# Kernel optimization log

Hardware: AMD Instinct MI355X
Metric: run time of the kernel (lower is better)

The kernel has to match this reference:

```python
import jax, jax.numpy as jnp
import numpy as np

N = 16384
IN_DIM = 128
OUT_DIM = 128
NUM_TYPES = 8


def setup_inputs() -> dict:
    key = jax.random.key(0)
    k1, k2, k3, k4 = jax.random.split(key, 4)
    x = jax.random.normal(k1, (N, IN_DIM), dtype=jnp.float32)
    node_types = jax.random.randint(k2, (N,), 0, NUM_TYPES, dtype=jnp.int32)
    adjacency = jax.random.uniform(k3, (N, N), dtype=jnp.float32)
    weight = jax.random.normal(k4, (NUM_TYPES, OUT_DIM, IN_DIM), dtype=jnp.float32)
    return {"x": x, "node_types": node_types, "adjacency": adjacency, "weight": weight}


def reference(x, node_types, adjacency, weight):
    # agg = A @ x : (N, in_dim)
    agg = jnp.matmul(adjacency, x)
    # Per-type projection: compute agg @ W[t].T for all types, then select
    # by node type. (N, T, out) intermediate is small (N*T*out floats).
    per_type = jnp.einsum("nd,tod->nto", agg, weight)  # (N, T, out)
    out = jnp.take_along_axis(per_type, node_types[:, None, None].astype(jnp.int32), axis=1)
    return out[:, 0, :]  # (N, out)
```

## Files before the change

kernel.cpp:

```cpp
#include <hip/hip_runtime.h>
#include <stdint.h>


#define N_NODES 16384
#define DIM     128
#define NTYPES  8
#define BM      64
#define BK      32
#define NIT     (N_NODES / BK)

typedef float  f32x4  __attribute__((ext_vector_type(4)));
typedef __bf16 bf16x8 __attribute__((ext_vector_type(8)));

__device__ __attribute__((aligned(16))) unsigned short g_xT[DIM * N_NODES];
__device__ __attribute__((aligned(16))) unsigned short g_Wb[NTYPES * DIM * DIM];

__device__ __forceinline__ unsigned int f2b(float f) {
    unsigned int u = __float_as_uint(f);
    u += 0x7FFFu + ((u >> 16) & 1u);
    return u >> 16;
}
#define BF_LO(u) __uint_as_float((unsigned int)(u) << 16)
#define BF_HI(u) __uint_as_float((unsigned int)(u) & 0xFFFF0000u)

__device__ __forceinline__ bf16x8 cvt8(const f32x4 lo, const f32x4 hi) {
    bf16x8 r;
    r[0] = (__bf16)lo[0]; r[1] = (__bf16)lo[1]; r[2] = (__bf16)lo[2]; r[3] = (__bf16)lo[3];
    r[4] = (__bf16)hi[0]; r[5] = (__bf16)hi[1]; r[6] = (__bf16)hi[2]; r[7] = (__bf16)hi[3];
    return r;
}


__global__ void prep_all(const float* __restrict__ x, const float* __restrict__ w) {
    const int tid = threadIdx.x;
    if (blockIdx.x < 64) {
        int n = blockIdx.x * 256 + tid;
        const float* row = x + (size_t)n * DIM;
#pragma unroll
        for (int d0 = 0; d0 < DIM; d0 += 4) {
            float4 v = *(const float4*)(row + d0);
            g_xT[(d0 + 0) * N_NODES + n] = (unsigned short)f2b(v.x);
            g_xT[(d0 + 1) * N_NODES + n] = (unsigned short)f2b(v.y);
            g_xT[(d0 + 2) * N_NODES + n] = (unsigned short)f2b(v.z);
            g_xT[(d0 + 3) * N_NODES + n] = (unsigned short)f2b(v.w);
        }
    } else {
        int base = ((blockIdx.x - 64) * 256 + tid) * 16;
#pragma unroll
        for (int j = 0; j < 4; ++j) {
            float4 v = *(const float4*)(w + base + j * 4);
            ushort4 o;
            o.x = (unsigned short)f2b(v.x); o.y = (unsigned short)f2b(v.y);
            o.z = (unsigned short)f2b(v.z); o.w = (unsigned short)f2b(v.w);
            *(ushort4*)(g_Wb + base + j * 4) = o;
        }
    }
}


#define ABYTES 8192
#define XBYTES 8192

#define GLOAD16(g, l) __builtin_amdgcn_global_load_lds(                         \
    (const __attribute__((address_space(1))) unsigned int*)(g),                 \
    (__attribute__((address_space(3))) unsigned int*)(l), 16, 0, 0)

#define COMPUTE(Ab, Xb) do {                                                    \
    f32x4 _lo = *(const f32x4*)((Ab) + aoE);                                    \
    f32x4 _hi = *(const f32x4*)((Ab) + aoO);                                    \
    bf16x8 _af = cvt8(_lo, _hi);                                                \
    bf16x8 _b0 = *(const bf16x8*)((Xb) + xbase);                                \
    bf16x8 _b1 = *(const bf16x8*)((Xb) + xbase + 1024);                         \
    bf16x8 _b2 = *(const bf16x8*)((Xb) + xbase + 2048);                         \
    bf16x8 _b3 = *(const bf16x8*)((Xb) + xbase + 3072);                         \
    acc0 = __builtin_amdgcn_mfma_f32_16x16x32_bf16(_af, _b0, acc0, 0, 0, 0);    \
    acc1 = __builtin_amdgcn_mfma_f32_16x16x32_bf16(_af, _b1, acc1, 0, 0, 0);    \
    acc2 = __builtin_amdgcn_mfma_f32_16x16x32_bf16(_af, _b2, acc2, 0, 0, 0);    \
    acc3 = __builtin_amdgcn_mfma_f32_16x16x32_bf16(_af, _b3, acc3, 0, 0, 0);    \
} while (0)

#define PHASE_I(Ac, Xc, Ai, Xi, VM) do {                                        \
    asm volatile("s_waitcnt vmcnt(" VM ")" ::: "memory");                       \
    __builtin_amdgcn_s_barrier();                                               \
    GLOAD16(gAp, (Ai) + wq);                                                    \
    GLOAD16(gXp, (Xi) + wq);                                                    \
    gAp += BK; gXp += BK;                                                       \
    COMPUTE(Ac, Xc);                                                            \
} while (0)

#define PHASE_N(Ac, Xc, VM) do {                                                \
    asm volatile("s_waitcnt vmcnt(" VM ")" ::: "memory");                       \
    __builtin_amdgcn_s_barrier();                                               \
    COMPUTE(Ac, Xc);                                                            \
} while (0)

__global__ __launch_bounds__(512, 1) void gconv_main(
    const float* __restrict__ adj,
    const int* __restrict__ types,
    float* __restrict__ out)
{
    __shared__ __align__(16) unsigned char lds[3 * ABYTES + 3 * XBYTES];
    unsigned char* A0 = lds;
    unsigned char* A1 = lds + ABYTES;
    unsigned char* A2 = lds + 2 * ABYTES;
    unsigned char* X0 = lds + 3 * ABYTES;
    unsigned char* X1 = X0 + XBYTES;
    unsigned char* X2 = X0 + 2 * XBYTES;

    const int tid  = threadIdx.x;
    const int w    = tid >> 6;
    const int l    = tid & 63;
    const int m0   = blockIdx.x * BM;

    const int mrow = (w & 3) * 16;
    const int ncol = (w >> 2) * 64;

    f32x4 acc0 = {}, acc1 = {}, acc2 = {}, acc3 = {};

    const float* gAp = adj + (size_t)(m0 + 8 * w + (l >> 3)) * N_NODES
                     + (((l & 7) ^ (l >> 3)) << 2);
    const unsigned short* gXp = g_xT + (size_t)(16 * w + (l >> 2)) * N_NODES
                              + (((l & 3) ^ ((l >> 3) & 3)) << 3);
    const int wq = w << 10;

    const int arow = mrow + (l & 15);
    const int ce   = (l >> 4) << 1;
    const int aoE  = arow * 128 + ((ce ^ (l & 7)) << 4);
    const int aoO  = arow * 128 + (((ce + 1) ^ (l & 7)) << 4);
    const int xph  = (l >> 4) ^ (((l & 15) >> 1) & 3);
    const int xbase = (ncol + (l & 15)) * 64 + (xph << 4);

    GLOAD16(gAp, A0 + wq); GLOAD16(gXp, X0 + wq); gAp += BK; gXp += BK;
    GLOAD16(gAp, A1 + wq); GLOAD16(gXp, X1 + wq); gAp += BK; gXp += BK;

    for (int j = 0; j < 169; ++j) {
        PHASE_I(A0, X0, A2, X2, "2");
        PHASE_I(A1, X1, A0, X0, "2");
        PHASE_I(A2, X2, A1, X1, "2");
    }
    PHASE_I(A0, X0, A2, X2, "2");
    PHASE_I(A1, X1, A0, X0, "2");
    PHASE_I(A2, X2, A1, X1, "2");
    PHASE_N(A0, X0, "2");
    PHASE_N(A1, X1, "0");
    __syncthreads();

    float* agg = (float*)lds;
#pragma unroll
    for (int r = 0; r < 4; ++r) {
        const int gr = (mrow + (l >> 4) * 4 + r) * 132 + ncol + (l & 15);
        agg[gr +  0] = acc0[r];
        agg[gr + 16] = acc1[r];
        agg[gr + 32] = acc2[r];
        agg[gr + 48] = acc3[r];
    }
    __syncthreads();

    const int rbase = w * 8;
    for (int rr = 0; rr < 8; ++rr) {
        const int rw = rbase + rr;
        const int nn = m0 + rw;
        const int ty = types[nn];
        const unsigned short* Wt = g_Wb + ty * (DIM * DIM);
        const int o0 = l * 2;
        const float* aggRow = agg + rw * 132;
        float s0 = 0.f, s1 = 0.f;
#pragma unroll
        for (int d0 = 0; d0 < DIM; d0 += 8) {
            float4 ga = *(const float4*)(aggRow + d0);
            float4 gb = *(const float4*)(aggRow + d0 + 4);
            uint4 wa = *(const uint4*)(Wt + o0 * DIM + d0);
            uint4 wb = *(const uint4*)(Wt + (o0 + 1) * DIM + d0);
            s0 += ga.x * BF_LO(wa.x) + ga.y * BF_HI(wa.x) + ga.z * BF_LO(wa.y) + ga.w * BF_HI(wa.y);
            s0 += gb.x * BF_LO(wa.z) + gb.y * BF_HI(wa.z) + gb.z * BF_LO(wa.w) + gb.w * BF_HI(wa.w);
            s1 += ga.x * BF_LO(wb.x) + ga.y * BF_HI(wb.x) + ga.z * BF_LO(wb.y) + ga.w * BF_HI(wb.y);
            s1 += gb.x * BF_LO(wb.z) + gb.y * BF_HI(wb.z) + gb.z * BF_LO(wb.w) + gb.w * BF_HI(wb.w);
        }
        float2 res; res.x = s0; res.y = s1;
        *(float2*)(out + (size_t)nn * DIM + o0) = res;
    }
}


extern "C" void kernel_launch(void* const* d_in, const int* in_sizes, int n_in,
                              void* d_out, int out_size, void* d_ws, size_t ws_size,
                              hipStream_t stream) {
    const float* x     = (const float*)d_in[0];
    const int*   types = (const int*)d_in[1];
    const float* adj   = (const float*)d_in[2];
    const float* wt    = (const float*)d_in[3];
    float* out = (float*)d_out;

    hipLaunchKernelGGL(prep_all, dim3(96), dim3(256), 0, stream, x, wt);
    hipLaunchKernelGGL(gconv_main, dim3(N_NODES / BM), dim3(512), 0, stream, adj, types, out);
}
```

Before: 350.8 us.

## Widen K tile to 128 with double-buffered LDS and fewer barriers

```diff
diff --git a/kernel.cpp b/kernel.cpp
--- a/kernel.cpp
+++ b/kernel.cpp
@@ -6,8 +6,8 @@
 #define DIM     128
 #define NTYPES  8
 #define BM      64
-#define BK      32
-#define NIT     (N_NODES / BK)
+#define BK      128
+#define NT_K    (N_NODES / BK)
 
 typedef float  f32x4  __attribute__((ext_vector_type(4)));
 typedef __bf16 bf16x8 __attribute__((ext_vector_type(8)));
@@ -58,40 +58,49 @@
 }
 
 
-#define ABYTES 8192
-#define XBYTES 8192
+#define ABYTES 32768
+#define XBYTES 32768
 
 #define GLOAD16(g, l) __builtin_amdgcn_global_load_lds(                         \
     (const __attribute__((address_space(1))) unsigned int*)(g),                 \
     (__attribute__((address_space(3))) unsigned int*)(l), 16, 0, 0)
 
-#define COMPUTE(Ab, Xb) do {                                                    \
-    f32x4 _lo = *(const f32x4*)((Ab) + aoE);                                    \
-    f32x4 _hi = *(const f32x4*)((Ab) + aoO);                                    \
-    bf16x8 _af = cvt8(_lo, _hi);                                                \
-    bf16x8 _b0 = *(const bf16x8*)((Xb) + xbase);                                \
-    bf16x8 _b1 = *(const bf16x8*)((Xb) + xbase + 1024);                         \
-    bf16x8 _b2 = *(const bf16x8*)((Xb) + xbase + 2048);                         \
-    bf16x8 _b3 = *(const bf16x8*)((Xb) + xbase + 3072);                         \
-    acc0 = __builtin_amdgcn_mfma_f32_16x16x32_bf16(_af, _b0, acc0, 0, 0, 0);    \
-    acc1 = __builtin_amdgcn_mfma_f32_16x16x32_bf16(_af, _b1, acc1, 0, 0, 0);    \
-    acc2 = __builtin_amdgcn_mfma_f32_16x16x32_bf16(_af, _b2, acc2, 0, 0, 0);    \
-    acc3 = __builtin_amdgcn_mfma_f32_16x16x32_bf16(_af, _b3, acc3, 0, 0, 0);    \
-} while (0)
-
-#define PHASE_I(Ac, Xc, Ai, Xi, VM) do {                                        \
-    asm volatile("s_waitcnt vmcnt(" VM ")" ::: "memory");                       \
-    __builtin_amdgcn_s_barrier();                                               \
-    GLOAD16(gAp, (Ai) + wq);                                                    \
-    GLOAD16(gXp, (Xi) + wq);                                                    \
-    gAp += BK; gXp += BK;                                                       \
-    COMPUTE(Ac, Xc);                                                            \
-} while (0)
-
-#define PHASE_N(Ac, Xc, VM) do {                                                \
-    asm volatile("s_waitcnt vmcnt(" VM ")" ::: "memory");                       \
-    __builtin_amdgcn_s_barrier();                                               \
-    COMPUTE(Ac, Xc);                                                            \
+#define DMA8(Ab, Xb) do {                                                       \
+    GLOAD16(gA0, (Ab) + wq);          GLOAD16(gA1, (Ab) +  8192 + wq);          \
+    GLOAD16(gA2, (Ab) + 16384 + wq);  GLOAD16(gA3, (Ab) + 24576 + wq);          \
+    GLOAD16(gX0, (Xb) + wq);          GLOAD16(gX1, (Xb) +  8192 + wq);          \
+    GLOAD16(gX2, (Xb) + 16384 + wq);  GLOAD16(gX3, (Xb) + 24576 + wq);          \
+    gA0 += BK; gA1 += BK; gA2 += BK; gA3 += BK;                                 \
+    gX0 += BK; gX1 += BK; gX2 += BK; gX3 += BK;                                 \
+} while (0)
+
+#define KSUB(Ab, Xb, kc, xo) do {                                               \
+    f32x4 _e = *(const f32x4*)((Ab) + aoE + (kc) * 128);                        \
+    f32x4 _o = *(const f32x4*)((Ab) + aoO + (kc) * 128);                        \
+    bf16x8 _a = cvt8(_e, _o);                                                   \
+    bf16x8 _b0 = *(const bf16x8*)((Xb) + (xo));                                 \
+    bf16x8 _b1 = *(const bf16x8*)((Xb) + (xo) + 4096);                          \
+    bf16x8 _b2 = *(const bf16x8*)((Xb) + (xo) + 8192);                          \
+    bf16x8 _b3 = *(const bf16x8*)((Xb) + (xo) + 12288);                         \
+    acc0 = __builtin_amdgcn_mfma_f32_16x16x32_bf16(_a, _b0, acc0, 0, 0, 0);     \
+    acc1 = __builtin_amdgcn_mfma_f32_16x16x32_bf16(_a, _b1, acc1, 0, 0, 0);     \
+    acc2 = __builtin_amdgcn_mfma_f32_16x16x32_bf16(_a, _b2, acc2, 0, 0, 0);     \
+    acc3 = __builtin_amdgcn_mfma_f32_16x16x32_bf16(_a, _b3, acc3, 0, 0, 0);     \
+} while (0)
+
+#define COMPUTE(Ab, Xb) do {        \
+    KSUB(Ab, Xb, 0, xo0);           \
+    KSUB(Ab, Xb, 1, xo1);           \
+    KSUB(Ab, Xb, 2, xo2);           \
+    KSUB(Ab, Xb, 3, xo3);           \
+} while (0)
+
+#define PHASE_I(Ac, Xc) do {                                 \
+    asm volatile("s_waitcnt vmcnt(8)" ::: "memory");         \
+    __builtin_amdgcn_s_barrier();                            \
+    COMPUTE(Ac, Xc);                                         \
+    asm volatile("s_barrier" ::: "memory");                  \
+    DMA8(Ac, Xc);                                            \
 } while (0)
 
 __global__ __launch_bounds__(512, 1) void gconv_main(
@@ -99,13 +108,11 @@
     const int* __restrict__ types,
     float* __restrict__ out)
 {
-    __shared__ __align__(16) unsigned char lds[3 * ABYTES + 3 * XBYTES];
-    unsigned char* A0 = lds;
-    unsigned char* A1 = lds + ABYTES;
-    unsigned char* A2 = lds + 2 * ABYTES;
-    unsigned char* X0 = lds + 3 * ABYTES;
-    unsigned char* X1 = X0 + XBYTES;
-    unsigned char* X2 = X0 + 2 * XBYTES;
+    __shared__ __align__(16) unsigned char lds[2 * (ABYTES + XBYTES)];
+    unsigned char* Ab0 = lds;
+    unsigned char* Ab1 = lds + ABYTES;
+    unsigned char* Xb0 = lds + 2 * ABYTES;
+    unsigned char* Xb1 = Xb0 + XBYTES;
 
     const int tid  = threadIdx.x;
     const int w    = tid >> 6;
@@ -117,42 +124,52 @@
 
     f32x4 acc0 = {}, acc1 = {}, acc2 = {}, acc3 = {};
 
-    const float* gAp = adj + (size_t)(m0 + 8 * w + (l >> 3)) * N_NODES
-                     + (((l & 7) ^ (l >> 3)) << 2);
-    const unsigned short* gXp = g_xT + (size_t)(16 * w + (l >> 2)) * N_NODES
-                              + (((l & 3) ^ ((l >> 3) & 3)) << 3);
+    const int arw = 2 * w + (l >> 5);
+    const float* gA0 = adj + (size_t)(m0 + arw) * N_NODES
+                     + (((l & 31) ^ (arw & 7)) << 2);
+    const float* gA1 = gA0 + (size_t)16 * N_NODES;
+    const float* gA2 = gA0 + (size_t)32 * N_NODES;
+    const float* gA3 = gA0 + (size_t)48 * N_NODES;
+    const int xdw = 4 * w + (l >> 4);
+    const unsigned short* gX0 = g_xT + (size_t)xdw * N_NODES
+                              + (((l & 15) ^ (xdw & 7)) << 3);
+    const unsigned short* gX1 = gX0 + (size_t)32 * N_NODES;
+    const unsigned short* gX2 = gX0 + (size_t)64 * N_NODES;
+    const unsigned short* gX3 = gX0 + (size_t)96 * N_NODES;
     const int wq = w << 10;
 
-    const int arow = mrow + (l & 15);
-    const int ce   = (l >> 4) << 1;
-    const int aoE  = arow * 128 + ((ce ^ (l & 7)) << 4);
-    const int aoO  = arow * 128 + (((ce + 1) ^ (l & 7)) << 4);
-    const int xph  = (l >> 4) ^ (((l & 15) >> 1) & 3);
-    const int xbase = (ncol + (l & 15)) * 64 + (xph << 4);
-
-    GLOAD16(gAp, A0 + wq); GLOAD16(gXp, X0 + wq); gAp += BK; gXp += BK;
-    GLOAD16(gAp, A1 + wq); GLOAD16(gXp, X1 + wq); gAp += BK; gXp += BK;
-
-    for (int j = 0; j < 169; ++j) {
-        PHASE_I(A0, X0, A2, X2, "2");
-        PHASE_I(A1, X1, A0, X0, "2");
-        PHASE_I(A2, X2, A1, X1, "2");
-    }
-    PHASE_I(A0, X0, A2, X2, "2");
-    PHASE_I(A1, X1, A0, X0, "2");
-    PHASE_I(A2, X2, A1, X1, "2");
-    PHASE_N(A0, X0, "2");
-    PHASE_N(A1, X1, "0");
+    const int r    = mrow + (l & 15);
+    const int aoE  = r * 512 + ((((l >> 4) * 2)     ^ (l & 7)) << 4);
+    const int aoO  = r * 512 + ((((l >> 4) * 2 + 1) ^ (l & 7)) << 4);
+    const int dd   = (ncol + (l & 15)) * 256;
+    const int xo0  = dd + ((( 0 + (l >> 4)) ^ (l & 7)) << 4);
+    const int xo1  = dd + ((( 4 + (l >> 4)) ^ (l & 7)) << 4);
+    const int xo2  = dd + ((( 8 + (l >> 4)) ^ (l & 7)) << 4);
+    const int xo3  = dd + (((12 + (l >> 4)) ^ (l & 7)) << 4);
+
+    DMA8(Ab0, Xb0);
+    DMA8(Ab1, Xb1);
+
+    for (int i = 0; i < 63; ++i) {
+        PHASE_I(Ab0, Xb0);
+        PHASE_I(Ab1, Xb1);
+    }
+    asm volatile("s_waitcnt vmcnt(8)" ::: "memory");
+    __builtin_amdgcn_s_barrier();
+    COMPUTE(Ab0, Xb0);
+    asm volatile("s_waitcnt vmcnt(0)" ::: "memory");
+    __builtin_amdgcn_s_barrier();
+    COMPUTE(Ab1, Xb1);
     __syncthreads();
 
     float* agg = (float*)lds;
 #pragma unroll
-    for (int r = 0; r < 4; ++r) {
-        const int gr = (mrow + (l >> 4) * 4 + r) * 132 + ncol + (l & 15);
-        agg[gr +  0] = acc0[r];
-        agg[gr + 16] = acc1[r];
-        agg[gr + 32] = acc2[r];
-        agg[gr + 48] = acc3[r];
+    for (int rr = 0; rr < 4; ++rr) {
+        const int gr = (mrow + (l >> 4) * 4 + rr) * 132 + ncol + (l & 15);
+        agg[gr +  0] = acc0[rr];
+        agg[gr + 16] = acc1[rr];
+        agg[gr + 32] = acc2[rr];
+        agg[gr + 48] = acc3[rr];
     }
     __syncthreads();
 
```

New measurement: 310.4 us. 1.13x faster.

## Load adjacency tiles directly into registers with larger K tiles and 32x32 MFMA

Applied to the files above, without the earlier changes.

```diff
diff --git a/kernel.cpp b/kernel.cpp
--- a/kernel.cpp
+++ b/kernel.cpp
@@ -6,10 +6,11 @@
 #define DIM     128
 #define NTYPES  8
 #define BM      64
-#define BK      32
-#define NIT     (N_NODES / BK)
+#define BK      128
+#define NT_K    (N_NODES / BK)
 
 typedef float  f32x4  __attribute__((ext_vector_type(4)));
+typedef float  f32x16 __attribute__((ext_vector_type(16)));
 typedef __bf16 bf16x8 __attribute__((ext_vector_type(8)));
 
 __device__ __attribute__((aligned(16))) unsigned short g_xT[DIM * N_NODES];
@@ -58,106 +59,148 @@
 }
 
 
-#define ABYTES 8192
-#define XBYTES 8192
+#define XBYTES 32768
 
 #define GLOAD16(g, l) __builtin_amdgcn_global_load_lds(                         \
     (const __attribute__((address_space(1))) unsigned int*)(g),                 \
     (__attribute__((address_space(3))) unsigned int*)(l), 16, 0, 0)
 
-#define COMPUTE(Ab, Xb) do {                                                    \
-    f32x4 _lo = *(const f32x4*)((Ab) + aoE);                                    \
-    f32x4 _hi = *(const f32x4*)((Ab) + aoO);                                    \
-    bf16x8 _af = cvt8(_lo, _hi);                                                \
-    bf16x8 _b0 = *(const bf16x8*)((Xb) + xbase);                                \
-    bf16x8 _b1 = *(const bf16x8*)((Xb) + xbase + 1024);                         \
-    bf16x8 _b2 = *(const bf16x8*)((Xb) + xbase + 2048);                         \
-    bf16x8 _b3 = *(const bf16x8*)((Xb) + xbase + 3072);                         \
-    acc0 = __builtin_amdgcn_mfma_f32_16x16x32_bf16(_af, _b0, acc0, 0, 0, 0);    \
-    acc1 = __builtin_amdgcn_mfma_f32_16x16x32_bf16(_af, _b1, acc1, 0, 0, 0);    \
-    acc2 = __builtin_amdgcn_mfma_f32_16x16x32_bf16(_af, _b2, acc2, 0, 0, 0);    \
-    acc3 = __builtin_amdgcn_mfma_f32_16x16x32_bf16(_af, _b3, acc3, 0, 0, 0);    \
-} while (0)
-
-#define PHASE_I(Ac, Xc, Ai, Xi, VM) do {                                        \
-    asm volatile("s_waitcnt vmcnt(" VM ")" ::: "memory");                       \
-    __builtin_amdgcn_s_barrier();                                               \
-    GLOAD16(gAp, (Ai) + wq);                                                    \
-    GLOAD16(gXp, (Xi) + wq);                                                    \
-    gAp += BK; gXp += BK;                                                       \
-    COMPUTE(Ac, Xc);                                                            \
-} while (0)
-
-#define PHASE_N(Ac, Xc, VM) do {                                                \
-    asm volatile("s_waitcnt vmcnt(" VM ")" ::: "memory");                       \
-    __builtin_amdgcn_s_barrier();                                               \
-    COMPUTE(Ac, Xc);                                                            \
-} while (0)
-
-__global__ __launch_bounds__(512, 1) void gconv_main(
+#define ALOAD(reg, ptr, off) \
+    asm volatile("global_load_dwordx4 %0, %1, off offset:" #off : "=v"(reg) : "v"(ptr))
+
+#define ISSUE_A(P, pa) do {                          \
+    ALOAD(P##0,  pa,   0); ALOAD(P##1,  pa,  16);    \
+    ALOAD(P##2,  pa,  64); ALOAD(P##3,  pa,  80);    \
+    ALOAD(P##4,  pa, 128); ALOAD(P##5,  pa, 144);    \
+    ALOAD(P##6,  pa, 192); ALOAD(P##7,  pa, 208);    \
+    ALOAD(P##8,  pa, 256); ALOAD(P##9,  pa, 272);    \
+    ALOAD(P##10, pa, 320); ALOAD(P##11, pa, 336);    \
+    ALOAD(P##12, pa, 384); ALOAD(P##13, pa, 400);    \
+    ALOAD(P##14, pa, 448); ALOAD(P##15, pa, 464);    \
+    pa += 2 * BK;    \
+} while (0)
+
+#define ISSUE_X(Xb) do {                                          \
+    GLOAD16(gX0, (Xb) + 0 * 4096 + wq); gX0 += BK;                \
+    GLOAD16(gX1, (Xb) + 1 * 4096 + wq); gX1 += BK;                \
+    GLOAD16(gX2, (Xb) + 2 * 4096 + wq); gX2 += BK;                \
+    GLOAD16(gX3, (Xb) + 3 * 4096 + wq); gX3 += BK;                \
+    GLOAD16(gX4, (Xb) + 4 * 4096 + wq); gX4 += BK;                \
+    GLOAD16(gX5, (Xb) + 5 * 4096 + wq); gX5 += BK;                \
+    GLOAD16(gX6, (Xb) + 6 * 4096 + wq); gX6 += BK;                \
+    GLOAD16(gX7, (Xb) + 7 * 4096 + wq); gX7 += BK;                \
+} while (0)
+
+#define KS(rE, rO, Xb, xk) do {                                                 \
+    bf16x8 _a  = cvt8(rE, rO);                                                  \
+    bf16x8 _b0 = *(const bf16x8*)((Xb) + xb0 + (xk));                           \
+    bf16x8 _b1 = *(const bf16x8*)((Xb) + xb1 + (xk));                           \
+    accA = __builtin_amdgcn_mfma_f32_32x32x16_bf16(_a, _b0, accA, 0, 0, 0);     \
+    accB = __builtin_amdgcn_mfma_f32_32x32x16_bf16(_a, _b1, accB, 0, 0, 0);     \
+} while (0)
+
+#define COMPUTE(P, Xb) do {                  \
+    KS(P##0,  P##1,  Xb, xk0);               \
+    KS(P##2,  P##3,  Xb, xk1);               \
+    KS(P##4,  P##5,  Xb, xk2);               \
+    KS(P##6,  P##7,  Xb, xk3);               \
+    KS(P##8,  P##9,  Xb, xk4);               \
+    KS(P##10, P##11, Xb, xk5);               \
+    KS(P##12, P##13, Xb, xk6);               \
+    KS(P##14, P##15, Xb, xk7);               \
+} while (0)
+
+#define WAITV(N) do {                                            \
+    asm volatile("s_waitcnt vmcnt(" #N ")" ::: "memory");        \
+    __builtin_amdgcn_sched_barrier(0);                           \
+} while (0)
+
+__global__ __launch_bounds__(256, 1) void gconv_main(
     const float* __restrict__ adj,
     const int* __restrict__ types,
     float* __restrict__ out)
 {
-    __shared__ __align__(16) unsigned char lds[3 * ABYTES + 3 * XBYTES];
-    unsigned char* A0 = lds;
-    unsigned char* A1 = lds + ABYTES;
-    unsigned char* A2 = lds + 2 * ABYTES;
-    unsigned char* X0 = lds + 3 * ABYTES;
-    unsigned char* X1 = X0 + XBYTES;
-    unsigned char* X2 = X0 + 2 * XBYTES;
+    __shared__ __align__(16) unsigned char lds[2 * XBYTES];
+    unsigned char* Xb0 = lds;
+    unsigned char* Xb1 = lds + XBYTES;
 
     const int tid  = threadIdx.x;
     const int w    = tid >> 6;
     const int l    = tid & 63;
     const int m0   = blockIdx.x * BM;
 
-    const int mrow = (w & 3) * 16;
-    const int ncol = (w >> 2) * 64;
-
-    f32x4 acc0 = {}, acc1 = {}, acc2 = {}, acc3 = {};
-
-    const float* gAp = adj + (size_t)(m0 + 8 * w + (l >> 3)) * N_NODES
-                     + (((l & 7) ^ (l >> 3)) << 2);
-    const unsigned short* gXp = g_xT + (size_t)(16 * w + (l >> 2)) * N_NODES
-                              + (((l & 3) ^ ((l >> 3) & 3)) << 3);
+    const int mrow = (w & 1) * 32;
+    const int ncol = (w >> 1) * 64;
+
+    f32x16 accA = {}, accB = {};
+
+    const float* aBase = adj + (size_t)(m0 + mrow + (l & 31)) * N_NODES + ((l >> 5) << 3);
+    const float* pa0 = aBase;
+    const float* pa1 = aBase + BK;
+
+    const int xr = 4 * w + (l >> 4);
+    const unsigned short* gX0 = g_xT + (size_t)(  0 + xr) * N_NODES + (((l & 15) ^ (xr & 7)) << 3);
+    const unsigned short* gX1 = g_xT + (size_t)( 16 + xr) * N_NODES + (((l & 15) ^ (xr & 7)) << 3);
+    const unsigned short* gX2 = g_xT + (size_t)( 32 + xr) * N_NODES + (((l & 15) ^ (xr & 7)) << 3);
+    const unsigned short* gX3 = g_xT + (size_t)( 48 + xr) * N_NODES + (((l & 15) ^ (xr & 7)) << 3);
+    const unsigned short* gX4 = g_xT + (size_t)( 64 + xr) * N_NODES + (((l & 15) ^ (xr & 7)) << 3);
+    const unsigned short* gX5 = g_xT + (size_t)( 80 + xr) * N_NODES + (((l & 15) ^ (xr & 7)) << 3);
+    const unsigned short* gX6 = g_xT + (size_t)( 96 + xr) * N_NODES + (((l & 15) ^ (xr & 7)) << 3);
+    const unsigned short* gX7 = g_xT + (size_t)(112 + xr) * N_NODES + (((l & 15) ^ (xr & 7)) << 3);
     const int wq = w << 10;
 
-    const int arow = mrow + (l & 15);
-    const int ce   = (l >> 4) << 1;
-    const int aoE  = arow * 128 + ((ce ^ (l & 7)) << 4);
-    const int aoO  = arow * 128 + (((ce + 1) ^ (l & 7)) << 4);
-    const int xph  = (l >> 4) ^ (((l & 15) >> 1) & 3);
-    const int xbase = (ncol + (l & 15)) * 64 + (xph << 4);
-
-    GLOAD16(gAp, A0 + wq); GLOAD16(gXp, X0 + wq); gAp += BK; gXp += BK;
-    GLOAD16(gAp, A1 + wq); GLOAD16(gXp, X1 + wq); gAp += BK; gXp += BK;
-
-    for (int j = 0; j < 169; ++j) {
-        PHASE_I(A0, X0, A2, X2, "2");
-        PHASE_I(A1, X1, A0, X0, "2");
-        PHASE_I(A2, X2, A1, X1, "2");
-    }
-    PHASE_I(A0, X0, A2, X2, "2");
-    PHASE_I(A1, X1, A0, X0, "2");
-    PHASE_I(A2, X2, A1, X1, "2");
-    PHASE_N(A0, X0, "2");
-    PHASE_N(A1, X1, "0");
+    const int h  = l >> 5;
+    const int e  = l & 7;
+    const int xb0 = (ncol +  0 + (l & 31)) * 256;
+    const int xb1 = (ncol + 32 + (l & 31)) * 256;
+    const int xk0 = (( 0 + h) ^ e) << 4;
+    const int xk1 = (( 2 + h) ^ e) << 4;
+    const int xk2 = (( 4 + h) ^ e) << 4;
+    const int xk3 = (( 6 + h) ^ e) << 4;
+    const int xk4 = (( 8 + h) ^ e) << 4;
+    const int xk5 = ((10 + h) ^ e) << 4;
+    const int xk6 = ((12 + h) ^ e) << 4;
+    const int xk7 = ((14 + h) ^ e) << 4;
+
+    f32x4 p0, p1, p2, p3, p4, p5, p6, p7, p8, p9, p10, p11, p12, p13, p14, p15;
+    f32x4 q0, q1, q2, q3, q4, q5, q6, q7, q8, q9, q10, q11, q12, q13, q14, q15;
+
+    ISSUE_A(p, pa0); ISSUE_X(Xb0);
+    ISSUE_A(q, pa1); ISSUE_X(Xb1);
+
+    for (int i = 0; i < 63; ++i) {
+        WAITV(24);
+        __builtin_amdgcn_s_barrier();
+        COMPUTE(p, Xb0);
+        __builtin_amdgcn_sched_barrier(0);
+        __builtin_amdgcn_s_barrier();
+        ISSUE_A(p, pa0); ISSUE_X(Xb0);
+        WAITV(24);
+        __builtin_amdgcn_s_barrier();
+        COMPUTE(q, Xb1);
+        __builtin_amdgcn_sched_barrier(0);
+        __builtin_amdgcn_s_barrier();
+        ISSUE_A(q, pa1); ISSUE_X(Xb1);
+    }
+    WAITV(24);
+    __builtin_amdgcn_s_barrier();
+    COMPUTE(p, Xb0);
+    WAITV(0);
+    __builtin_amdgcn_s_barrier();
+    COMPUTE(q, Xb1);
     __syncthreads();
 
     float* agg = (float*)lds;
 #pragma unroll
-    for (int r = 0; r < 4; ++r) {
-        const int gr = (mrow + (l >> 4) * 4 + r) * 132 + ncol + (l & 15);
-        agg[gr +  0] = acc0[r];
-        agg[gr + 16] = acc1[r];
-        agg[gr + 32] = acc2[r];
-        agg[gr + 48] = acc3[r];
+    for (int rg = 0; rg < 16; ++rg) {
+        const int row = mrow + (rg & 3) + 8 * (rg >> 2) + 4 * (l >> 5);
+        agg[row * 132 + ncol +  0 + (l & 31)] = accA[rg];
+        agg[row * 132 + ncol + 32 + (l & 31)] = accB[rg];
     }
     __syncthreads();
 
-    const int rbase = w * 8;
-    for (int rr = 0; rr < 8; ++rr) {
+    const int rbase = w * 16;
+    for (int rr = 0; rr < 16; ++rr) {
         const int rw = rbase + rr;
         const int nn = m0 + rw;
         const int ty = types[nn];
@@ -192,5 +235,5 @@
     float* out = (float*)d_out;
 
     hipLaunchKernelGGL(prep_all, dim3(96), dim3(256), 0, stream, x, wt);
-    hipLaunchKernelGGL(gconv_main, dim3(N_NODES / BM), dim3(512), 0, stream, adj, types, out);
-}
+    hipLaunchKernelGGL(gconv_main, dim3(N_NODES / BM), dim3(256), 0, stream, adj, types, out);
+}
```

Result: slower. 408.3 us (+16.4%).

## Stage adjacency through registers as bf16 with larger K tile and 2x2 wave tiling

Applied to the files above, without the earlier changes.

```diff
diff --git a/kernel.cpp b/kernel.cpp
--- a/kernel.cpp
+++ b/kernel.cpp
@@ -6,10 +6,11 @@
 #define DIM     128
 #define NTYPES  8
 #define BM      64
-#define BK      32
-#define NIT     (N_NODES / BK)
+#define BK      128
+#define NT_K    (N_NODES / BK)
 
 typedef float  f32x4  __attribute__((ext_vector_type(4)));
+typedef __bf16 bf16x4 __attribute__((ext_vector_type(4)));
 typedef __bf16 bf16x8 __attribute__((ext_vector_type(8)));
 
 __device__ __attribute__((aligned(16))) unsigned short g_xT[DIM * N_NODES];
@@ -23,10 +24,9 @@
 #define BF_LO(u) __uint_as_float((unsigned int)(u) << 16)
 #define BF_HI(u) __uint_as_float((unsigned int)(u) & 0xFFFF0000u)
 
-__device__ __forceinline__ bf16x8 cvt8(const f32x4 lo, const f32x4 hi) {
-    bf16x8 r;
-    r[0] = (__bf16)lo[0]; r[1] = (__bf16)lo[1]; r[2] = (__bf16)lo[2]; r[3] = (__bf16)lo[3];
-    r[4] = (__bf16)hi[0]; r[5] = (__bf16)hi[1]; r[6] = (__bf16)hi[2]; r[7] = (__bf16)hi[3];
+__device__ __forceinline__ bf16x4 cvt4(const f32x4 v) {
+    bf16x4 r;
+    r[0] = (__bf16)v[0]; r[1] = (__bf16)v[1]; r[2] = (__bf16)v[2]; r[3] = (__bf16)v[3];
     return r;
 }
 
@@ -58,40 +58,73 @@
 }
 
 
-#define ABYTES 8192
-#define XBYTES 8192
+#define AB_BYTES 16384
+#define XB_BYTES 32768
 
 #define GLOAD16(g, l) __builtin_amdgcn_global_load_lds(                         \
     (const __attribute__((address_space(1))) unsigned int*)(g),                 \
     (__attribute__((address_space(3))) unsigned int*)(l), 16, 0, 0)
 
-#define COMPUTE(Ab, Xb) do {                                                    \
-    f32x4 _lo = *(const f32x4*)((Ab) + aoE);                                    \
-    f32x4 _hi = *(const f32x4*)((Ab) + aoO);                                    \
-    bf16x8 _af = cvt8(_lo, _hi);                                                \
-    bf16x8 _b0 = *(const bf16x8*)((Xb) + xbase);                                \
-    bf16x8 _b1 = *(const bf16x8*)((Xb) + xbase + 1024);                         \
-    bf16x8 _b2 = *(const bf16x8*)((Xb) + xbase + 2048);                         \
-    bf16x8 _b3 = *(const bf16x8*)((Xb) + xbase + 3072);                         \
-    acc0 = __builtin_amdgcn_mfma_f32_16x16x32_bf16(_af, _b0, acc0, 0, 0, 0);    \
-    acc1 = __builtin_amdgcn_mfma_f32_16x16x32_bf16(_af, _b1, acc1, 0, 0, 0);    \
-    acc2 = __builtin_amdgcn_mfma_f32_16x16x32_bf16(_af, _b2, acc2, 0, 0, 0);    \
-    acc3 = __builtin_amdgcn_mfma_f32_16x16x32_bf16(_af, _b3, acc3, 0, 0, 0);    \
-} while (0)
-
-#define PHASE_I(Ac, Xc, Ai, Xi, VM) do {                                        \
-    asm volatile("s_waitcnt vmcnt(" VM ")" ::: "memory");                       \
-    __builtin_amdgcn_s_barrier();                                               \
-    GLOAD16(gAp, (Ai) + wq);                                                    \
-    GLOAD16(gXp, (Xi) + wq);                                                    \
-    gAp += BK; gXp += BK;                                                       \
-    COMPUTE(Ac, Xc);                                                            \
-} while (0)
-
-#define PHASE_N(Ac, Xc, VM) do {                                                \
-    asm volatile("s_waitcnt vmcnt(" VM ")" ::: "memory");                       \
-    __builtin_amdgcn_s_barrier();                                               \
-    COMPUTE(Ac, Xc);                                                            \
+#define ALOADI(reg, ptr) \
+    asm volatile("global_load_dwordx4 %0, %1, off" : "=v"(reg) : "v"(ptr))
+
+#define ISSUE_AL(R0, R1, R2, R3) do {            \
+    ALOADI(R0, pA0); ALOADI(R1, pA1);            \
+    ALOADI(R2, pA2); ALOADI(R3, pA3);            \
+    pA0 += BK; pA1 += BK; pA2 += BK; pA3 += BK;  \
+} while (0)
+
+#define ISSUE_XD(Xb) do {                        \
+    GLOAD16(gX0, (Xb) + 0 * 8192 + wq);          \
+    GLOAD16(gX1, (Xb) + 1 * 8192 + wq);          \
+    GLOAD16(gX2, (Xb) + 2 * 8192 + wq);          \
+    GLOAD16(gX3, (Xb) + 3 * 8192 + wq);          \
+    gX0 += BK; gX1 += BK; gX2 += BK; gX3 += BK;  \
+} while (0)
+
+#define STOREA(As, R0, R1, R2, R3) do {          \
+    *(bf16x4*)((As) + aw0) = cvt4(R0);           \
+    *(bf16x4*)((As) + aw1) = cvt4(R1);           \
+    *(bf16x4*)((As) + aw2) = cvt4(R2);           \
+    *(bf16x4*)((As) + aw3) = cvt4(R3);           \
+} while (0)
+
+#define KS(Ab, Xb, off) do {                                                    \
+    bf16x8 a0_ = *(const bf16x8*)((Ab) + arA0 + (off));                         \
+    bf16x8 a1_ = *(const bf16x8*)((Ab) + arA1 + (off));                         \
+    bf16x8 b0_ = *(const bf16x8*)((Xb) + xB0 + (off));                          \
+    bf16x8 b1_ = *(const bf16x8*)((Xb) + xB1 + (off));                          \
+    acc00 = __builtin_amdgcn_mfma_f32_16x16x32_bf16(a0_, b0_, acc00, 0, 0, 0);  \
+    acc01 = __builtin_amdgcn_mfma_f32_16x16x32_bf16(a0_, b1_, acc01, 0, 0, 0);  \
+    acc10 = __builtin_amdgcn_mfma_f32_16x16x32_bf16(a1_, b0_, acc10, 0, 0, 0);  \
+    acc11 = __builtin_amdgcn_mfma_f32_16x16x32_bf16(a1_, b1_, acc11, 0, 0, 0);  \
+} while (0)
+
+#define COMPUTE(Ab, Xb) do {      \
+    KS(Ab, Xb, off0);             \
+    KS(Ab, Xb, off1);             \
+    KS(Ab, Xb, off2);             \
+    KS(Ab, Xb, off3);             \
+} while (0)
+
+#define WAITV(N) do {                                        \
+    asm volatile("s_waitcnt vmcnt(" #N ")" ::: "memory");    \
+    __builtin_amdgcn_sched_barrier(0);                       \
+} while (0)
+
+#define TOP(VM) do {                                                            \
+    asm volatile("s_waitcnt vmcnt(" #VM ") lgkmcnt(0)\n\ts_barrier" ::: "memory"); \
+    __builtin_amdgcn_sched_barrier(0);                                          \
+} while (0)
+
+#define PHASE(Ac, Xc, As, S0,S1,S2,S3, L0,L1,L2,L3, Xi) do {  \
+    TOP(8);                                                   \
+    COMPUTE(Ac, Xc);                                          \
+    __builtin_amdgcn_sched_barrier(0);                        \
+    WAITV(4);                                                 \
+    STOREA(As, S0, S1, S2, S3);                               \
+    ISSUE_AL(L0, L1, L2, L3);                                 \
+    ISSUE_XD(Xi);                                             \
 } while (0)
 
 __global__ __launch_bounds__(512, 1) void gconv_main(
@@ -99,60 +132,89 @@
     const int* __restrict__ types,
     float* __restrict__ out)
 {
-    __shared__ __align__(16) unsigned char lds[3 * ABYTES + 3 * XBYTES];
-    unsigned char* A0 = lds;
-    unsigned char* A1 = lds + ABYTES;
-    unsigned char* A2 = lds + 2 * ABYTES;
-    unsigned char* X0 = lds + 3 * ABYTES;
-    unsigned char* X1 = X0 + XBYTES;
-    unsigned char* X2 = X0 + 2 * XBYTES;
+    __shared__ __align__(16) unsigned char lds[3 * XB_BYTES + 2 * AB_BYTES];
+    unsigned char* X0 = lds;
+    unsigned char* X1 = lds + XB_BYTES;
+    unsigned char* X2 = lds + 2 * XB_BYTES;
+    unsigned char* Ab0 = lds + 3 * XB_BYTES;
+    unsigned char* Ab1 = Ab0 + AB_BYTES;
 
     const int tid  = threadIdx.x;
     const int w    = tid >> 6;
     const int l    = tid & 63;
     const int m0   = blockIdx.x * BM;
 
-    const int mrow = (w & 3) * 16;
-    const int ncol = (w >> 2) * 64;
-
-    f32x4 acc0 = {}, acc1 = {}, acc2 = {}, acc3 = {};
-
-    const float* gAp = adj + (size_t)(m0 + 8 * w + (l >> 3)) * N_NODES
-                     + (((l & 7) ^ (l >> 3)) << 2);
-    const unsigned short* gXp = g_xT + (size_t)(16 * w + (l >> 2)) * N_NODES
-                              + (((l & 3) ^ ((l >> 3) & 3)) << 3);
+    const int mrow = (w & 1) * 32;
+    const int ncol = (w >> 1) * 32;
+    const int h    = l >> 4;
+
+    f32x4 acc00 = {}, acc01 = {}, acc10 = {}, acc11 = {};
+
+    const int rj0 = w * 8 + 0 + (l >> 5);
+    const int rj1 = w * 8 + 2 + (l >> 5);
+    const int rj2 = w * 8 + 4 + (l >> 5);
+    const int rj3 = w * 8 + 6 + (l >> 5);
+    const float* pA0 = adj + (size_t)(m0 + rj0) * N_NODES + (l & 31) * 4;
+    const float* pA1 = adj + (size_t)(m0 + rj1) * N_NODES + (l & 31) * 4;
+    const float* pA2 = adj + (size_t)(m0 + rj2) * N_NODES + (l & 31) * 4;
+    const float* pA3 = adj + (size_t)(m0 + rj3) * N_NODES + (l & 31) * 4;
+    const int g_   = l & 31;
+    const int aw0 = rj0 * 256 + ((((g_ >> 1) ^ (rj0 & 7))) << 4) + ((g_ & 1) << 3);
+    const int aw1 = rj1 * 256 + ((((g_ >> 1) ^ (rj1 & 7))) << 4) + ((g_ & 1) << 3);
+    const int aw2 = rj2 * 256 + ((((g_ >> 1) ^ (rj2 & 7))) << 4) + ((g_ & 1) << 3);
+    const int aw3 = rj3 * 256 + ((((g_ >> 1) ^ (rj3 & 7))) << 4) + ((g_ & 1) << 3);
+
+    const int xdw = 4 * w + (l >> 4);
+    const unsigned short* gX0 = g_xT + (size_t)( 0 + xdw) * N_NODES + (((l & 15) ^ (xdw & 7)) << 3);
+    const unsigned short* gX1 = g_xT + (size_t)(32 + xdw) * N_NODES + (((l & 15) ^ (xdw & 7)) << 3);
+    const unsigned short* gX2 = g_xT + (size_t)(64 + xdw) * N_NODES + (((l & 15) ^ (xdw & 7)) << 3);
+    const unsigned short* gX3 = g_xT + (size_t)(96 + xdw) * N_NODES + (((l & 15) ^ (xdw & 7)) << 3);
     const int wq = w << 10;
 
-    const int arow = mrow + (l & 15);
-    const int ce   = (l >> 4) << 1;
-    const int aoE  = arow * 128 + ((ce ^ (l & 7)) << 4);
-    const int aoO  = arow * 128 + (((ce + 1) ^ (l & 7)) << 4);
-    const int xph  = (l >> 4) ^ (((l & 15) >> 1) & 3);
-    const int xbase = (ncol + (l & 15)) * 64 + (xph << 4);
-
-    GLOAD16(gAp, A0 + wq); GLOAD16(gXp, X0 + wq); gAp += BK; gXp += BK;
-    GLOAD16(gAp, A1 + wq); GLOAD16(gXp, X1 + wq); gAp += BK; gXp += BK;
-
-    for (int j = 0; j < 169; ++j) {
-        PHASE_I(A0, X0, A2, X2, "2");
-        PHASE_I(A1, X1, A0, X0, "2");
-        PHASE_I(A2, X2, A1, X1, "2");
-    }
-    PHASE_I(A0, X0, A2, X2, "2");
-    PHASE_I(A1, X1, A0, X0, "2");
-    PHASE_I(A2, X2, A1, X1, "2");
-    PHASE_N(A0, X0, "2");
-    PHASE_N(A1, X1, "0");
+    const int arA0 = (mrow +  0 + (l & 15)) * 256;
+    const int arA1 = (mrow + 16 + (l & 15)) * 256;
+    const int xB0  = (ncol +  0 + (l & 15)) * 256;
+    const int xB1  = (ncol + 16 + (l & 15)) * 256;
+    const int off0 = (( 0 + h) ^ (l & 7)) << 4;
+    const int off1 = (( 4 + h) ^ (l & 7)) << 4;
+    const int off2 = (( 8 + h) ^ (l & 7)) << 4;
+    const int off3 = ((12 + h) ^ (l & 7)) << 4;
+
+    f32x4 p0, p1, p2, p3, q0, q1, q2, q3;
+
+    ISSUE_AL(p0, p1, p2, p3);
+    ISSUE_XD(X0);
+    ISSUE_AL(q0, q1, q2, q3);
+    ISSUE_XD(X1);
+    WAITV(12);
+    STOREA(Ab0, p0, p1, p2, p3);
+
+    for (int i = 0; i < 21; ++i) {
+        PHASE(Ab0, X0, Ab1, q0,q1,q2,q3, p0,p1,p2,p3, X2);
+        PHASE(Ab1, X1, Ab0, p0,p1,p2,p3, q0,q1,q2,q3, X0);
+        PHASE(Ab0, X2, Ab1, q0,q1,q2,q3, p0,p1,p2,p3, X1);
+        PHASE(Ab1, X0, Ab0, p0,p1,p2,p3, q0,q1,q2,q3, X2);
+        PHASE(Ab0, X1, Ab1, q0,q1,q2,q3, p0,p1,p2,p3, X0);
+        PHASE(Ab1, X2, Ab0, p0,p1,p2,p3, q0,q1,q2,q3, X1);
+    }
+    TOP(8);
+    COMPUTE(Ab0, X0);
+    __builtin_amdgcn_sched_barrier(0);
+    WAITV(4);
+    STOREA(Ab1, q0, q1, q2, q3);
+    TOP(0);
+    COMPUTE(Ab1, X1);
     __syncthreads();
 
     float* agg = (float*)lds;
 #pragma unroll
     for (int r = 0; r < 4; ++r) {
-        const int gr = (mrow + (l >> 4) * 4 + r) * 132 + ncol + (l & 15);
-        agg[gr +  0] = acc0[r];
-        agg[gr + 16] = acc1[r];
-        agg[gr + 32] = acc2[r];
-        agg[gr + 48] = acc3[r];
+        const int r0 = (mrow +  0 + h * 4 + r) * 132 + ncol + (l & 15);
+        const int r1 = (mrow + 16 + h * 4 + r) * 132 + ncol + (l & 15);
+        agg[r0 +  0] = acc00[r];
+        agg[r0 + 16] = acc01[r];
+        agg[r1 +  0] = acc10[r];
+        agg[r1 + 16] = acc11[r];
     }
     __syncthreads();
 
```

Measured after the change: 302.5 us. -13.8%, faster.
